# Kernel tuning notes

Hardware: AMD Instinct MI355X
Metric: run time of the kernel (lower is better)

The kernel has to match this reference:

```python
import jax, jax.numpy as jnp
import numpy as np

N = 50000
E = 600000
OB_DIM = 128
H = 128
P_OUT = 8


def _glorot(key, fan_in, fan_out):
    lim = float(np.sqrt(6.0 / (fan_in + fan_out)))
    return jax.random.uniform(key, (fan_in, fan_out), jnp.float32, -lim, lim)


def setup_inputs() -> dict:
    key = jax.random.key(0)
    ks = jax.random.split(key, 16)
    x = jax.random.normal(ks[0], (N, OB_DIM), jnp.float32)
    edge_index = jax.random.randint(ks[1], (2, E), 0, N, jnp.int64)
    dims = [(OB_DIM, H), (H, H), (H, P_OUT), (OB_DIM, H), (H, H), (H, 1)]
    names = ["p1", "p2", "p3", "v1", "v2", "v3"]
    inp = {"x": x, "edge_index": edge_index}
    for i, (nm, (fi, fo)) in enumerate(zip(names, dims)):
        inp["W" + nm] = _glorot(ks[2 + i], fi, fo)
        inp["b" + nm] = jnp.zeros((fo,), jnp.float32)
    return inp


def _gcn_norm(edge_index, n):
    # add self-loops, symmetric normalization deg^{-1/2} A_hat deg^{-1/2}
    loops = jnp.arange(n, dtype=edge_index.dtype)
    src = jnp.concatenate([edge_index[0], loops])
    dst = jnp.concatenate([edge_index[1], loops])
    deg = jax.ops.segment_sum(jnp.ones_like(dst, jnp.float32), dst, num_segments=n)
    dinv = jax.lax.rsqrt(jnp.maximum(deg, 1.0))
    norm = dinv[src] * dinv[dst]  # [E+N]
    return src, dst, norm


def _gcn_conv(x, W, b, src, dst, norm, n):
    h = x @ W                      # [N, out]
    msg = h[src] * norm[:, None]   # gather + scale, [E+N, out]
    out = jax.ops.segment_sum(msg, dst, num_segments=n)
    return out + b


def reference(x, edge_index, Wp1, bp1, Wp2, bp2, Wp3, bp3, Wv1, bv1, Wv2, bv2, Wv3, bv3):
    n = x.shape[0]
    src, dst, norm = _gcn_norm(edge_index, n)
    # policy branch
    a = jax.nn.relu(_gcn_conv(x, Wp1, bp1, src, dst, norm, n))
    a = jax.nn.relu(_gcn_conv(a, Wp2, bp2, src, dst, norm, n))
    action_logits = _gcn_conv(a, Wp3, bp3, src, dst, norm, n)  # Categorical logits
    # value branch
    v = jax.nn.relu(_gcn_conv(x, Wv1, bv1, src, dst, norm, n))
    v = jax.nn.relu(_gcn_conv(v, Wv2, bv2, src, dst, norm, n))
    v = _gcn_conv(v, Wv3, bv3, src, dst, norm, n)
    return action_logits, v
```

## Files before the change

### kernel.cpp

```cpp
#include <hip/hip_runtime.h>

#define NN 50000
#define NE 600000

typedef unsigned short ushort_t;
typedef ushort_t ushortx8 __attribute__((ext_vector_type(8)));
typedef ushort_t ushortx4 __attribute__((ext_vector_type(4)));
typedef short bf16x8 __attribute__((ext_vector_type(8)));
typedef float f32x4 __attribute__((ext_vector_type(4)));
typedef int intx2 __attribute__((ext_vector_type(2)));
typedef float fltx4 __attribute__((ext_vector_type(4)));

__device__ __forceinline__ float bf2f(ushort_t u) {
    union { unsigned int i; float f; } c;
    c.i = ((unsigned int)u) << 16;
    return c.f;
}
__device__ __forceinline__ ushort_t f2bf(float f) {
    union { float f; unsigned int i; } c;
    c.f = f;
    unsigned int u = c.i;
    unsigned int r = u + 0x7FFFu + ((u >> 16) & 1u);
    return (ushort_t)(r >> 16);
}
__device__ __forceinline__ unsigned cvtpk(float lo, float hi) {
    unsigned r;
    asm("v_cvt_pk_bf16_f32 %0, %1, %2" : "=v"(r) : "v"(lo), "v"(hi));
    return r;
}

__global__ void k_xbf(const float* __restrict__ X, ushort_t* __restrict__ XB) {
    size_t i = (size_t)blockIdx.x * 256 + threadIdx.x;
    const float4* X4 = (const float4*)X;
    float4 a = X4[i * 2], b = X4[i * 2 + 1];
    union { unsigned u[4]; ushortx8 v; } cv;
    cv.u[0] = cvtpk(a.x, a.y);
    cv.u[1] = cvtpk(a.z, a.w);
    cv.u[2] = cvtpk(b.x, b.y);
    cv.u[3] = cvtpk(b.z, b.w);
    __builtin_nontemporal_store(cv.v, (ushortx8*)XB + i);
}


__global__ void k_count(const int* __restrict__ ei, int* __restrict__ cnt) {
    int e = blockIdx.x * 256 + threadIdx.x;
    if (e < NE) {
        int d = __builtin_nontemporal_load(ei + NE + e);
        atomicAdd(&cnt[d], 1);
    }
}

__global__ void k_scan1(const int* __restrict__ cnt, int* __restrict__ rowptr,
                        int* __restrict__ bsum, float* __restrict__ dinv) {
    __shared__ int s[256];
    int t = threadIdx.x;
    int i = blockIdx.x * 256 + t;
    int v = (i < NN) ? cnt[i] : 0;
    if (i < NN) dinv[i] = rsqrtf(1.0f + (float)v);
    s[t] = v;
    __syncthreads();
    for (int d = 1; d < 256; d <<= 1) {
        int tmp = (t >= d) ? s[t - d] : 0;
        __syncthreads();
        s[t] += tmp;
        __syncthreads();
    }
    if (i < NN) rowptr[i] = s[t] - v;
    if (t == 255) bsum[blockIdx.x] = s[255];
}

__global__ void k_scan2_prep(int* __restrict__ bsum, int* __restrict__ boff, int nb,
                             const float* __restrict__ Wp1, const float* __restrict__ Wv1,
                             const float* __restrict__ Wp2, const float* __restrict__ Wv2,
                             ushort_t* __restrict__ Wt1, ushort_t* __restrict__ Wt2p,
                             ushort_t* __restrict__ Wt2v) {
    int b = blockIdx.x, t = threadIdx.x;
    if (b < 128) {
        int idx = b * 256 + t;
        int n = idx >> 7, k = idx & 127;
        float v = (n < 128) ? Wp1[k * 128 + n] : Wv1[k * 128 + (n - 128)];
        Wt1[n * 128 + k] = f2bf(v);
    } else if (b < 192) {
        int idx = (b - 128) * 256 + t;
        int n = idx >> 7, k = idx & 127;
        Wt2p[n * 128 + k] = f2bf(Wp2[k * 128 + n]);
    } else if (b < 256) {
        int idx = (b - 192) * 256 + t;
        int n = idx >> 7, k = idx & 127;
        Wt2v[n * 128 + k] = f2bf(Wv2[k * 128 + n]);
    } else {
        __shared__ int s[256];
        int v = (t < nb) ? bsum[t] : 0;
        s[t] = v;
        __syncthreads();
        for (int d = 1; d < 256; d <<= 1) {
            int tmp = (t >= d) ? s[t - d] : 0;
            __syncthreads();
            s[t] += tmp;
            __syncthreads();
        }
        boff[t] = s[t] - v;
    }
}

__global__ void k_scan3rc(const int* __restrict__ rowptr, const int* __restrict__ cnt,
                          const int* __restrict__ boff, int2* __restrict__ rc) {
    int i = blockIdx.x * 256 + threadIdx.x;
    if (i < NN) {
        int2 v;
        v.x = rowptr[i] + boff[blockIdx.x];
        v.y = cnt[i];
        rc[i] = v;
    }
}

__global__ void k_fill(const int* __restrict__ ei, const int2* __restrict__ rc,
                       int* __restrict__ fill, const float* __restrict__ dinv,
                       int2* __restrict__ edges) {
    int e = blockIdx.x * 256 + threadIdx.x;
    if (e < NE) {
        int s = __builtin_nontemporal_load(ei + e);
        int d = __builtin_nontemporal_load(ei + NE + e);
        int pos = rc[d].x + atomicAdd(&fill[d], 1);
        int2 pr;
        pr.x = s;
        pr.y = __float_as_int(dinv[s] * dinv[d]);
        edges[pos] = pr;
    }
}

__global__ __launch_bounds__(256) void k_agg128(const ushort_t* __restrict__ H,
                                                ushort_t* __restrict__ OUT,
                                                const float* __restrict__ dinv,
                                                const int2* __restrict__ rc,
                                                const int2* __restrict__ edges) {
    int wv = threadIdx.x >> 6;
    int l = threadIdx.x & 63;
    int i = blockIdx.x * 4 + wv;
    if (i >= NN) return;
    int t2 = l >> 4, q = l & 15;
    const ushortx8* H8 = (const ushortx8*)H;

    float a0[8] = {}, a1[8] = {};
    float di = dinv[i];
    float ws = (t2 == 0) ? di * di : 0.f;
    ushortx8 hv = H8[(size_t)i * 16 + q];
#pragma unroll
    for (int k = 0; k < 8; ++k) a0[k] = ws * bf2f(hv[k]);

    int2 rcv = rc[i];
    int st = rcv.x, n = rcv.y;

    for (int j = t2; j < n; j += 16) {
        int idx[4];
        float w[4];
#pragma unroll
        for (int s = 0; s < 4; ++s) {
            int jj = j + 4 * s;
            bool valid = jj < n;
            intx2 em = __builtin_nontemporal_load(
                (const intx2*)edges + (valid ? st + jj : st));
            idx[s] = valid ? em.x : i;
            w[s] = valid ? __int_as_float(em.y) : 0.f;
        }
        ushortx8 hh[4];
#pragma unroll
        for (int s = 0; s < 4; ++s) hh[s] = H8[(size_t)idx[s] * 16 + q];
#pragma unroll
        for (int k = 0; k < 8; ++k) a0[k] += w[0] * bf2f(hh[0][k]);
#pragma unroll
        for (int k = 0; k < 8; ++k) a1[k] += w[1] * bf2f(hh[1][k]);
#pragma unroll
        for (int k = 0; k < 8; ++k) a0[k] += w[2] * bf2f(hh[2][k]);
#pragma unroll
        for (int k = 0; k < 8; ++k) a1[k] += w[3] * bf2f(hh[3][k]);
    }
#pragma unroll
    for (int k = 0; k < 8; ++k) a0[k] += a1[k];
#pragma unroll
    for (int k = 0; k < 8; ++k) {
        a0[k] += __shfl_xor(a0[k], 16, 64);
        a0[k] += __shfl_xor(a0[k], 32, 64);
    }
    if (l < 16) {
        ushortx8 o = {f2bf(a0[0]), f2bf(a0[1]), f2bf(a0[2]), f2bf(a0[3]),
                      f2bf(a0[4]), f2bf(a0[5]), f2bf(a0[6]), f2bf(a0[7])};
        __builtin_nontemporal_store(o, (ushortx8*)OUT + (size_t)i * 16 + q);
    }
}

__global__ __launch_bounds__(256) void k_agg256(const ushort_t* __restrict__ H,
                                                ushort_t* __restrict__ OUT,
                                                const float* __restrict__ dinv,
                                                const int2* __restrict__ rc,
                                                const int2* __restrict__ edges) {
    int wv = threadIdx.x >> 6;
    int l = threadIdx.x & 63;
    int i = blockIdx.x * 4 + wv;
    if (i >= NN) return;
    int h = l >> 5, q = l & 31;
    const ushortx8* H8 = (const ushortx8*)H;

    float a0[8] = {}, a1[8] = {};
    float di = dinv[i];
    float ws = (h == 0) ? di * di : 0.f;
    ushortx8 hv = H8[(size_t)i * 32 + q];
#pragma unroll
    for (int k = 0; k < 8; ++k) a0[k] = ws * bf2f(hv[k]);

    int2 rcv = rc[i];
    int st = rcv.x, n = rcv.y;

    for (int j = h; j < n; j += 8) {
        int idx[4];
        float w[4];
#pragma unroll
        for (int s = 0; s < 4; ++s) {
            int jj = j + 2 * s;
            bool valid = jj < n;
            intx2 em = __builtin_nontemporal_load(
                (const intx2*)edges + (valid ? st + jj : st));
            idx[s] = valid ? em.x : i;
            w[s] = valid ? __int_as_float(em.y) : 0.f;
        }
        ushortx8 hh[4];
#pragma unroll
        for (int s = 0; s < 4; ++s) hh[s] = H8[(size_t)idx[s] * 32 + q];
#pragma unroll
        for (int k = 0; k < 8; ++k) a0[k] += w[0] * bf2f(hh[0][k]);
#pragma unroll
        for (int k = 0; k < 8; ++k) a1[k] += w[1] * bf2f(hh[1][k]);
#pragma unroll
        for (int k = 0; k < 8; ++k) a0[k] += w[2] * bf2f(hh[2][k]);
#pragma unroll
        for (int k = 0; k < 8; ++k) a1[k] += w[3] * bf2f(hh[3][k]);
    }
#pragma unroll
    for (int k = 0; k < 8; ++k) a0[k] += a1[k];
#pragma unroll
    for (int k = 0; k < 8; ++k) a0[k] += __shfl_xor(a0[k], 32, 64);

    if (h == 0) {
        ushortx8 o = {f2bf(a0[0]), f2bf(a0[1]), f2bf(a0[2]), f2bf(a0[3]),
                      f2bf(a0[4]), f2bf(a0[5]), f2bf(a0[6]), f2bf(a0[7])};
        __builtin_nontemporal_store(o, (ushortx8*)OUT + (size_t)i * 32 + q);
    }
}

__global__ __launch_bounds__(256) void k_gemm1(const ushort_t* __restrict__ A,
                                               const ushort_t* __restrict__ Wt1,
                                               const float* __restrict__ bL,
                                               const float* __restrict__ bH,
                                               ushort_t* __restrict__ C, int nrows) {
    __shared__ ushort_t Wl[256 * 128];
    int t = threadIdx.x;
    const ushortx8* Wg = (const ushortx8*)Wt1;
#pragma unroll
    for (int i = 0; i < 16; ++i) {
        int c = i * 256 + t;
        int row = c >> 4, slot = c & 15;
        int db = row * 256 + ((slot * 16) ^ ((row & 7) << 4));
        *(ushortx8*)((char*)Wl + db) = Wg[c];
    }
    __syncthreads();

    int w = t >> 6, l = t & 63, m = l & 15, g = l >> 4;
    int r0 = blockIdx.x * 64 + w * 16;
    if (r0 >= nrows) return;

    const ushort_t* Arow = A + (size_t)(r0 + m) * 128;
    bf16x8 af[4];
#pragma unroll
    for (int kk = 0; kk < 4; ++kk) af[kk] = *(const bf16x8*)(Arow + kk * 32 + g * 8);

    f32x4 acc[16];
#pragma unroll
    for (int nt = 0; nt < 16; ++nt) acc[nt] = (f32x4){0.f, 0.f, 0.f, 0.f};
    int sw = (m & 7) << 4;
#pragma unroll
    for (int nt = 0; nt < 16; ++nt) {
        const char* Wb = (const char*)Wl + (nt * 16 + m) * 256;
#pragma unroll
        for (int kk = 0; kk < 4; ++kk) {
            bf16x8 wf = *(const bf16x8*)(Wb + ((kk * 64 + g * 16) ^ sw));
            acc[nt] = __builtin_amdgcn_mfma_f32_16x16x32_bf16(wf, af[kk], acc[nt], 0, 0, 0);
        }
    }
#pragma unroll
    for (int nt = 0; nt < 16; ++nt) {
        const float* bb = (nt < 8) ? (bL + nt * 16 + g * 4) : (bH + (nt - 8) * 16 + g * 4);
        float4 bv = *(const float4*)bb;
        ushortx4 o = {f2bf(fmaxf(acc[nt][0] + bv.x, 0.f)),
                      f2bf(fmaxf(acc[nt][1] + bv.y, 0.f)),
                      f2bf(fmaxf(acc[nt][2] + bv.z, 0.f)),
                      f2bf(fmaxf(acc[nt][3] + bv.w, 0.f))};
        *(ushortx4*)(C + (size_t)(r0 + m) * 256 + nt * 16 + g * 4) = o;
    }
}

__global__ __launch_bounds__(256) void k_gemm2(const ushort_t* __restrict__ A,
                                               const ushort_t* __restrict__ Wp,
                                               const ushort_t* __restrict__ Wv,
                                               const float* __restrict__ bL,
                                               const float* __restrict__ bH,
                                               ushort_t* __restrict__ C, int nrows) {
    __shared__ ushort_t Wl[2 * 128 * 128];
    int t = threadIdx.x;
    const ushortx8* Wgp = (const ushortx8*)Wp;
    const ushortx8* Wgv = (const ushortx8*)Wv;
#pragma unroll
    for (int i = 0; i < 8; ++i) {
        int c = i * 256 + t;
        int row = c >> 4, slot = c & 15;
        int db = row * 256 + ((slot * 16) ^ ((row & 7) << 4));
        *(ushortx8*)((char*)Wl + db) = Wgp[c];
        *(ushortx8*)((char*)Wl + 32768 + db) = Wgv[c];
    }
    __syncthreads();

    int w = t >> 6, l = t & 63, m = l & 15, g = l >> 4;
    int r0 = blockIdx.x * 64 + w * 16;
    if (r0 >= nrows) return;

    const ushort_t* Arow = A + (size_t)(r0 + m) * 256;
    bf16x8 alo[4], ahi[4];
#pragma unroll
    for (int kk = 0; kk < 4; ++kk) {
        alo[kk] = *(const bf16x8*)(Arow + kk * 32 + g * 8);
        ahi[kk] = *(const bf16x8*)(Arow + 128 + kk * 32 + g * 8);
    }

    f32x4 accp[8], accv[8];
#pragma unroll
    for (int nt = 0; nt < 8; ++nt) {
        accp[nt] = (f32x4){0.f, 0.f, 0.f, 0.f};
        accv[nt] = (f32x4){0.f, 0.f, 0.f, 0.f};
    }
    int sw = (m & 7) << 4;
#pragma unroll
    for (int nt = 0; nt < 8; ++nt) {
        const char* Wbp = (const char*)Wl + (nt * 16 + m) * 256;
        const char* Wbv = Wbp + 32768;
#pragma unroll
        for (int kk = 0; kk < 4; ++kk) {
            int off = (kk * 64 + g * 16) ^ sw;
            bf16x8 wfp = *(const bf16x8*)(Wbp + off);
            accp[nt] = __builtin_amdgcn_mfma_f32_16x16x32_bf16(wfp, alo[kk], accp[nt], 0, 0, 0);
            bf16x8 wfv = *(const bf16x8*)(Wbv + off);
            accv[nt] = __builtin_amdgcn_mfma_f32_16x16x32_bf16(wfv, ahi[kk], accv[nt], 0, 0, 0);
        }
    }
#pragma unroll
    for (int nt = 0; nt < 8; ++nt) {
        float4 bp = *(const float4*)(bL + nt * 16 + g * 4);
        float4 bv = *(const float4*)(bH + nt * 16 + g * 4);
        ushortx4 op = {f2bf(fmaxf(accp[nt][0] + bp.x, 0.f)),
                       f2bf(fmaxf(accp[nt][1] + bp.y, 0.f)),
                       f2bf(fmaxf(accp[nt][2] + bp.z, 0.f)),
                       f2bf(fmaxf(accp[nt][3] + bp.w, 0.f))};
        ushortx4 ov = {f2bf(fmaxf(accv[nt][0] + bv.x, 0.f)),
                       f2bf(fmaxf(accv[nt][1] + bv.y, 0.f)),
                       f2bf(fmaxf(accv[nt][2] + bv.z, 0.f)),
                       f2bf(fmaxf(accv[nt][3] + bv.w, 0.f))};
        *(ushortx4*)(C + (size_t)(r0 + m) * 256 + nt * 16 + g * 4) = op;
        *(ushortx4*)(C + (size_t)(r0 + m) * 256 + 128 + nt * 16 + g * 4) = ov;
    }
}

__global__ __launch_bounds__(256) void k_small(const ushort_t* __restrict__ F2,
                                               const float* __restrict__ Wp3,
                                               const float* __restrict__ Wv3,
                                               float* __restrict__ FS) {
    __shared__ float Wp[8 * 128];
    __shared__ float Wv[128];
    int t = threadIdx.x;
    for (int j = t; j < 1024; j += 256) {
        int k = j >> 3, c = j & 7;
        Wp[c * 128 + k] = Wp3[j];
    }
    if (t < 128) Wv[t] = Wv3[t];
    __syncthreads();
    int row = blockIdx.x * 256 + t;
    if (row >= NN) return;
    const ushortx8* F8 = (const ushortx8*)F2;
    size_t base = (size_t)row * 32;
    float acc[9] = {};
#pragma unroll 2
    for (int kc = 0; kc < 16; ++kc) {
        ushortx8 p = F8[base + kc];
        ushortx8 v = F8[base + 16 + kc];
#pragma unroll
        for (int jj = 0; jj < 8; ++jj) {
            float pv = bf2f(p[jj]);
            int k = kc * 8 + jj;
#pragma unroll
            for (int c = 0; c < 8; ++c) acc[c] += pv * Wp[c * 128 + k];
            acc[8] += bf2f(v[jj]) * Wv[k];
        }
    }
    float4* FSo = (float4*)(FS + (size_t)row * 12);
    float4 o0 = {acc[0], acc[1], acc[2], acc[3]};
    float4 o1 = {acc[4], acc[5], acc[6], acc[7]};
    float4 o2 = {acc[8], 0.f, 0.f, 0.f};
    FSo[0] = o0; FSo[1] = o1; FSo[2] = o2;
}

__global__ void k_agg9(const float* __restrict__ FS, float* __restrict__ out_logits,
                       float* __restrict__ out_v, const float* __restrict__ bp3,
                       const float* __restrict__ bv3, const float* __restrict__ dinv,
                       const int2* __restrict__ rc, const int2* __restrict__ edges) {
    int i = blockIdx.x * 256 + threadIdx.x;
    if (i >= NN) return;
    float di = dinv[i];
    float w0 = di * di;
    const float4* F = (const float4*)FS;
    size_t b0 = (size_t)i * 3;
    float4 x0 = F[b0], x1 = F[b0 + 1], x2 = F[b0 + 2];
    float a[9];
    a[0] = w0 * x0.x; a[1] = w0 * x0.y; a[2] = w0 * x0.z; a[3] = w0 * x0.w;
    a[4] = w0 * x1.x; a[5] = w0 * x1.y; a[6] = w0 * x1.z; a[7] = w0 * x1.w;
    a[8] = w0 * x2.x;
    int2 rcv = rc[i];
    int st = rcv.x, n = rcv.y;
    for (int j = 0; j < n; ++j) {
        int2 e = edges[st + j];
        float w = __int_as_float(e.y);
        size_t sb = (size_t)e.x * 3;
        float4 y0 = F[sb], y1 = F[sb + 1], y2 = F[sb + 2];
        a[0] += w * y0.x; a[1] += w * y0.y; a[2] += w * y0.z; a[3] += w * y0.w;
        a[4] += w * y1.x; a[5] += w * y1.y; a[6] += w * y1.z; a[7] += w * y1.w;
        a[8] += w * y2.x;
    }
    float4 bpa = *(const float4*)bp3;
    float4 bpb = *(const float4*)(bp3 + 4);
    fltx4 o0 = {a[0] + bpa.x, a[1] + bpa.y, a[2] + bpa.z, a[3] + bpa.w};
    fltx4 o1 = {a[4] + bpb.x, a[5] + bpb.y, a[6] + bpb.z, a[7] + bpb.w};
    __builtin_nontemporal_store(o0, (fltx4*)out_logits + (size_t)i * 2);
    __builtin_nontemporal_store(o1, (fltx4*)out_logits + (size_t)i * 2 + 1);
    __builtin_nontemporal_store(a[8] + bv3[0], out_v + i);
}

extern "C" void kernel_launch(void* const* d_in, const int* in_sizes, int n_in,
                              void* d_out, int out_size, void* d_ws, size_t ws_size,
                              hipStream_t stream) {
    const float* x   = (const float*)d_in[0];
    const int*   ei  = (const int*)d_in[1];
    const float* Wp1 = (const float*)d_in[2],  *bp1 = (const float*)d_in[3];
    const float* Wp2 = (const float*)d_in[4],  *bp2 = (const float*)d_in[5];
    const float* Wp3 = (const float*)d_in[6],  *bp3 = (const float*)d_in[7];
    const float* Wv1 = (const float*)d_in[8],  *bv1 = (const float*)d_in[9];
    const float* Wv2 = (const float*)d_in[10], *bv2 = (const float*)d_in[11];
    const float* Wv3 = (const float*)d_in[12], *bv3 = (const float*)d_in[13];
    float* out_logits = (float*)d_out;
    float* out_v = (float*)d_out + (size_t)NN * 8;

    char* w = (char*)d_ws;
    auto alloc = [&](size_t bytes) {
        char* p = w;
        w += (bytes + 255) & ~(size_t)255;
        return p;
    };
    int*      cntfill = (int*)alloc((size_t)2 * NN * 4);
    int*      cnt    = cntfill;
    int*      fill   = cntfill + NN;
    int*      rowptr = (int*)alloc(NN * 4);
    int*      bsum   = (int*)alloc(256 * 4);
    int*      boff   = (int*)alloc(256 * 4);
    float*    dinv   = (float*)alloc(NN * 4);
    int2*     rc     = (int2*)alloc((size_t)NN * 8);
    int2*     edges  = (int2*)alloc((size_t)NE * 8);
    ushort_t* Wt1    = (ushort_t*)alloc(256 * 128 * 2);
    ushort_t* Wt2p   = (ushort_t*)alloc(128 * 128 * 2);
    ushort_t* Wt2v   = (ushort_t*)alloc(128 * 128 * 2);
    ushort_t* xb     = (ushort_t*)alloc((size_t)NN * 128 * 2);
    ushort_t* ag0    = (ushort_t*)alloc((size_t)NN * 128 * 2);
    ushort_t* f1b    = (ushort_t*)alloc((size_t)NN * 256 * 2);
    ushort_t* ag1    = (ushort_t*)alloc((size_t)NN * 256 * 2);
    ushort_t* f2b    = (ushort_t*)alloc((size_t)NN * 256 * 2);
    float*    fs     = (float*)alloc((size_t)NN * 12 * 4);

    const int NB = (NN + 255) / 256;
    const int EB = (NE + 255) / 256;
    const int GB = (NN + 63) / 64;
    const int AB = NN / 4;

    k_xbf<<<3125, 256, 0, stream>>>(x, xb);
    (void)hipMemsetAsync(cntfill, 0, (size_t)2 * NN * 4, stream);
    k_count<<<EB, 256, 0, stream>>>(ei, cnt);
    k_scan1<<<NB, 256, 0, stream>>>(cnt, rowptr, bsum, dinv);
    k_scan2_prep<<<257, 256, 0, stream>>>(bsum, boff, NB, Wp1, Wv1, Wp2, Wv2,
                                          Wt1, Wt2p, Wt2v);
    k_scan3rc<<<NB, 256, 0, stream>>>(rowptr, cnt, boff, rc);
    k_fill<<<EB, 256, 0, stream>>>(ei, rc, fill, dinv, edges);

    k_agg128<<<AB, 256, 0, stream>>>(xb, ag0, dinv, rc, edges);
    k_gemm1<<<GB, 256, 0, stream>>>(ag0, Wt1, bp1, bv1, f1b, NN);
    k_agg256<<<AB, 256, 0, stream>>>(f1b, ag1, dinv, rc, edges);
    k_gemm2<<<GB, 256, 0, stream>>>(ag1, Wt2p, Wt2v, bp2, bv2, f2b, NN);
    k_small<<<NB, 256, 0, stream>>>(f2b, Wp3, Wv3, fs);
    k_agg9<<<NB, 256, 0, stream>>>(fs, out_logits, out_v, bp3, bv3, dinv, rc, edges);
}
```

Measured before the change: 219.3 us.

## Fuse final small GEMM into gemm2, merge preprocessing kernels, compact edge list

```diff
diff --git a/kernel.cpp b/kernel.cpp
--- a/kernel.cpp
+++ b/kernel.cpp
@@ -8,7 +8,6 @@
 typedef ushort_t ushortx4 __attribute__((ext_vector_type(4)));
 typedef short bf16x8 __attribute__((ext_vector_type(8)));
 typedef float f32x4 __attribute__((ext_vector_type(4)));
-typedef int intx2 __attribute__((ext_vector_type(2)));
 typedef float fltx4 __attribute__((ext_vector_type(4)));
 
 __device__ __forceinline__ float bf2f(ushort_t u) {
@@ -29,24 +28,25 @@
     return r;
 }
 
-__global__ void k_xbf(const float* __restrict__ X, ushort_t* __restrict__ XB) {
-    size_t i = (size_t)blockIdx.x * 256 + threadIdx.x;
-    const float4* X4 = (const float4*)X;
-    float4 a = X4[i * 2], b = X4[i * 2 + 1];
-    union { unsigned u[4]; ushortx8 v; } cv;
-    cv.u[0] = cvtpk(a.x, a.y);
-    cv.u[1] = cvtpk(a.z, a.w);
-    cv.u[2] = cvtpk(b.x, b.y);
-    cv.u[3] = cvtpk(b.z, b.w);
-    __builtin_nontemporal_store(cv.v, (ushortx8*)XB + i);
-}
-
-
-__global__ void k_count(const int* __restrict__ ei, int* __restrict__ cnt) {
-    int e = blockIdx.x * 256 + threadIdx.x;
-    if (e < NE) {
-        int d = __builtin_nontemporal_load(ei + NE + e);
-        atomicAdd(&cnt[d], 1);
+__global__ void k_pre(const float* __restrict__ X, ushort_t* __restrict__ XB,
+                      const int* __restrict__ ei, int* __restrict__ cnt) {
+    int b = blockIdx.x;
+    if (b < 3125) {
+        size_t i = (size_t)b * 256 + threadIdx.x;
+        const float4* X4 = (const float4*)X;
+        float4 a = X4[i * 2], c4 = X4[i * 2 + 1];
+        union { unsigned u[4]; ushortx8 v; } cv;
+        cv.u[0] = cvtpk(a.x, a.y);
+        cv.u[1] = cvtpk(a.z, a.w);
+        cv.u[2] = cvtpk(c4.x, c4.y);
+        cv.u[3] = cvtpk(c4.z, c4.w);
+        __builtin_nontemporal_store(cv.v, (ushortx8*)XB + i);
+    } else {
+        int e = (b - 3125) * 256 + threadIdx.x;
+        if (e < NE) {
+            int d = __builtin_nontemporal_load(ei + NE + e);
+            atomicAdd(&cnt[d], 1);
+        }
     }
 }
 
@@ -115,17 +115,13 @@
 }
 
 __global__ void k_fill(const int* __restrict__ ei, const int2* __restrict__ rc,
-                       int* __restrict__ fill, const float* __restrict__ dinv,
-                       int2* __restrict__ edges) {
+                       int* __restrict__ fill, int* __restrict__ edges) {
     int e = blockIdx.x * 256 + threadIdx.x;
     if (e < NE) {
         int s = __builtin_nontemporal_load(ei + e);
         int d = __builtin_nontemporal_load(ei + NE + e);
         int pos = rc[d].x + atomicAdd(&fill[d], 1);
-        int2 pr;
-        pr.x = s;
-        pr.y = __float_as_int(dinv[s] * dinv[d]);
-        edges[pos] = pr;
+        edges[pos] = s;
     }
 }
 
@@ -133,7 +129,7 @@
                                                 ushort_t* __restrict__ OUT,
                                                 const float* __restrict__ dinv,
                                                 const int2* __restrict__ rc,
-                                                const int2* __restrict__ edges) {
+                                                const int* __restrict__ edges) {
     int wv = threadIdx.x >> 6;
     int l = threadIdx.x & 63;
     int i = blockIdx.x * 4 + wv;
@@ -158,10 +154,9 @@
         for (int s = 0; s < 4; ++s) {
             int jj = j + 4 * s;
             bool valid = jj < n;
-            intx2 em = __builtin_nontemporal_load(
-                (const intx2*)edges + (valid ? st + jj : st));
-            idx[s] = valid ? em.x : i;
-            w[s] = valid ? __int_as_float(em.y) : 0.f;
+            int em = __builtin_nontemporal_load(edges + (valid ? st + jj : st));
+            idx[s] = valid ? em : i;
+            w[s] = valid ? dinv[em] * di : 0.f;
         }
         ushortx8 hh[4];
 #pragma unroll
@@ -193,7 +188,7 @@
                                                 ushort_t* __restrict__ OUT,
                                                 const float* __restrict__ dinv,
                                                 const int2* __restrict__ rc,
-                                                const int2* __restrict__ edges) {
+                                                const int* __restrict__ edges) {
     int wv = threadIdx.x >> 6;
     int l = threadIdx.x & 63;
     int i = blockIdx.x * 4 + wv;
@@ -218,10 +213,9 @@
         for (int s = 0; s < 4; ++s) {
             int jj = j + 2 * s;
             bool valid = jj < n;
-            intx2 em = __builtin_nontemporal_load(
-                (const intx2*)edges + (valid ? st + jj : st));
-            idx[s] = valid ? em.x : i;
-            w[s] = valid ? __int_as_float(em.y) : 0.f;
+            int em = __builtin_nontemporal_load(edges + (valid ? st + jj : st));
+            idx[s] = valid ? em : i;
+            w[s] = valid ? dinv[em] * di : 0.f;
         }
         ushortx8 hh[4];
 #pragma unroll
@@ -298,13 +292,16 @@
     }
 }
 
-__global__ __launch_bounds__(256) void k_gemm2(const ushort_t* __restrict__ A,
-                                               const ushort_t* __restrict__ Wp,
-                                               const ushort_t* __restrict__ Wv,
-                                               const float* __restrict__ bL,
-                                               const float* __restrict__ bH,
-                                               ushort_t* __restrict__ C, int nrows) {
+__global__ __launch_bounds__(256) void k_gemm2s(const ushort_t* __restrict__ A,
+                                                const ushort_t* __restrict__ Wp,
+                                                const ushort_t* __restrict__ Wv,
+                                                const float* __restrict__ bL,
+                                                const float* __restrict__ bH,
+                                                const float* __restrict__ Wp3,
+                                                const float* __restrict__ Wv3,
+                                                float* __restrict__ FS, int nrows) {
     __shared__ ushort_t Wl[2 * 128 * 128];
+    __shared__ float W3c[9][128];
     int t = threadIdx.x;
     const ushortx8* Wgp = (const ushortx8*)Wp;
     const ushortx8* Wgv = (const ushortx8*)Wv;
@@ -316,6 +313,10 @@
         *(ushortx8*)((char*)Wl + db) = Wgp[c];
         *(ushortx8*)((char*)Wl + 32768 + db) = Wgv[c];
     }
+    for (int jj = t; jj < 1152; jj += 256) {
+        int c = jj >> 7, k = jj & 127;
+        W3c[c][k] = (c < 8) ? Wp3[k * 8 + c] : Wv3[k];
+    }
     __syncthreads();
 
     int w = t >> 6, l = t & 63, m = l & 15, g = l >> 4;
@@ -350,65 +351,55 @@
             accv[nt] = __builtin_amdgcn_mfma_f32_16x16x32_bf16(wfv, ahi[kk], accv[nt], 0, 0, 0);
         }
     }
+
+    float rp[8][4], rv[8][4];
 #pragma unroll
     for (int nt = 0; nt < 8; ++nt) {
         float4 bp = *(const float4*)(bL + nt * 16 + g * 4);
         float4 bv = *(const float4*)(bH + nt * 16 + g * 4);
-        ushortx4 op = {f2bf(fmaxf(accp[nt][0] + bp.x, 0.f)),
-                       f2bf(fmaxf(accp[nt][1] + bp.y, 0.f)),
-                       f2bf(fmaxf(accp[nt][2] + bp.z, 0.f)),
-                       f2bf(fmaxf(accp[nt][3] + bp.w, 0.f))};
-        ushortx4 ov = {f2bf(fmaxf(accv[nt][0] + bv.x, 0.f)),
-                       f2bf(fmaxf(accv[nt][1] + bv.y, 0.f)),
-                       f2bf(fmaxf(accv[nt][2] + bv.z, 0.f)),
-                       f2bf(fmaxf(accv[nt][3] + bv.w, 0.f))};
-        *(ushortx4*)(C + (size_t)(r0 + m) * 256 + nt * 16 + g * 4) = op;
-        *(ushortx4*)(C + (size_t)(r0 + m) * 256 + 128 + nt * 16 + g * 4) = ov;
-    }
-}
-
-__global__ __launch_bounds__(256) void k_small(const ushort_t* __restrict__ F2,
-                                               const float* __restrict__ Wp3,
-                                               const float* __restrict__ Wv3,
-                                               float* __restrict__ FS) {
-    __shared__ float Wp[8 * 128];
-    __shared__ float Wv[128];
-    int t = threadIdx.x;
-    for (int j = t; j < 1024; j += 256) {
-        int k = j >> 3, c = j & 7;
-        Wp[c * 128 + k] = Wp3[j];
-    }
-    if (t < 128) Wv[t] = Wv3[t];
-    __syncthreads();
-    int row = blockIdx.x * 256 + t;
-    if (row >= NN) return;
-    const ushortx8* F8 = (const ushortx8*)F2;
-    size_t base = (size_t)row * 32;
-    float acc[9] = {};
-#pragma unroll 2
-    for (int kc = 0; kc < 16; ++kc) {
-        ushortx8 p = F8[base + kc];
-        ushortx8 v = F8[base + 16 + kc];
-#pragma unroll
-        for (int jj = 0; jj < 8; ++jj) {
-            float pv = bf2f(p[jj]);
-            int k = kc * 8 + jj;
-#pragma unroll
-            for (int c = 0; c < 8; ++c) acc[c] += pv * Wp[c * 128 + k];
-            acc[8] += bf2f(v[jj]) * Wv[k];
-        }
-    }
-    float4* FSo = (float4*)(FS + (size_t)row * 12);
-    float4 o0 = {acc[0], acc[1], acc[2], acc[3]};
-    float4 o1 = {acc[4], acc[5], acc[6], acc[7]};
-    float4 o2 = {acc[8], 0.f, 0.f, 0.f};
-    FSo[0] = o0; FSo[1] = o1; FSo[2] = o2;
+        rp[nt][0] = fmaxf(accp[nt][0] + bp.x, 0.f);
+        rp[nt][1] = fmaxf(accp[nt][1] + bp.y, 0.f);
+        rp[nt][2] = fmaxf(accp[nt][2] + bp.z, 0.f);
+        rp[nt][3] = fmaxf(accp[nt][3] + bp.w, 0.f);
+        rv[nt][0] = fmaxf(accv[nt][0] + bv.x, 0.f);
+        rv[nt][1] = fmaxf(accv[nt][1] + bv.y, 0.f);
+        rv[nt][2] = fmaxf(accv[nt][2] + bv.z, 0.f);
+        rv[nt][3] = fmaxf(accv[nt][3] + bv.w, 0.f);
+    }
+
+    float ps[9] = {};
+#pragma unroll
+    for (int c = 0; c < 8; ++c) {
+#pragma unroll
+        for (int nt = 0; nt < 8; ++nt) {
+            float4 w4 = *(const float4*)&W3c[c][nt * 16 + g * 4];
+            ps[c] += rp[nt][0] * w4.x + rp[nt][1] * w4.y + rp[nt][2] * w4.z + rp[nt][3] * w4.w;
+        }
+    }
+#pragma unroll
+    for (int nt = 0; nt < 8; ++nt) {
+        float4 w4 = *(const float4*)&W3c[8][nt * 16 + g * 4];
+        ps[8] += rv[nt][0] * w4.x + rv[nt][1] * w4.y + rv[nt][2] * w4.z + rv[nt][3] * w4.w;
+    }
+#pragma unroll
+    for (int c = 0; c < 9; ++c) {
+        ps[c] += __shfl_xor(ps[c], 16, 64);
+        ps[c] += __shfl_xor(ps[c], 32, 64);
+    }
+    if (g == 0) {
+        float* o = FS + (size_t)(r0 + m) * 12;
+        fltx4 o0 = {ps[0], ps[1], ps[2], ps[3]};
+        fltx4 o1 = {ps[4], ps[5], ps[6], ps[7]};
+        __builtin_nontemporal_store(o0, (fltx4*)o);
+        __builtin_nontemporal_store(o1, (fltx4*)o + 1);
+        __builtin_nontemporal_store(ps[8], o + 8);
+    }
 }
 
 __global__ void k_agg9(const float* __restrict__ FS, float* __restrict__ out_logits,
                        float* __restrict__ out_v, const float* __restrict__ bp3,
                        const float* __restrict__ bv3, const float* __restrict__ dinv,
-                       const int2* __restrict__ rc, const int2* __restrict__ edges) {
+                       const int2* __restrict__ rc, const int* __restrict__ edges) {
     int i = blockIdx.x * 256 + threadIdx.x;
     if (i >= NN) return;
     float di = dinv[i];
@@ -423,9 +414,9 @@
     int2 rcv = rc[i];
     int st = rcv.x, n = rcv.y;
     for (int j = 0; j < n; ++j) {
-        int2 e = edges[st + j];
-        float w = __int_as_float(e.y);
-        size_t sb = (size_t)e.x * 3;
+        int e = edges[st + j];
+        float w = dinv[e] * di;
+        size_t sb = (size_t)e * 3;
         float4 y0 = F[sb], y1 = F[sb + 1], y2 = F[sb + 2];
         a[0] += w * y0.x; a[1] += w * y0.y; a[2] += w * y0.z; a[3] += w * y0.w;
         a[4] += w * y1.x; a[5] += w * y1.y; a[6] += w * y1.z; a[7] += w * y1.w;
@@ -468,7 +459,7 @@
     int*      boff   = (int*)alloc(256 * 4);
     float*    dinv   = (float*)alloc(NN * 4);
     int2*     rc     = (int2*)alloc((size_t)NN * 8);
-    int2*     edges  = (int2*)alloc((size_t)NE * 8);
+    int*      edges  = (int*)alloc((size_t)NE * 4);
     ushort_t* Wt1    = (ushort_t*)alloc(256 * 128 * 2);
     ushort_t* Wt2p   = (ushort_t*)alloc(128 * 128 * 2);
     ushort_t* Wt2v   = (ushort_t*)alloc(128 * 128 * 2);
@@ -476,7 +467,6 @@
     ushort_t* ag0    = (ushort_t*)alloc((size_t)NN * 128 * 2);
     ushort_t* f1b    = (ushort_t*)alloc((size_t)NN * 256 * 2);
     ushort_t* ag1    = (ushort_t*)alloc((size_t)NN * 256 * 2);
-    ushort_t* f2b    = (ushort_t*)alloc((size_t)NN * 256 * 2);
     float*    fs     = (float*)alloc((size_t)NN * 12 * 4);
 
     const int NB = (NN + 255) / 256;
@@ -484,19 +474,17 @@
     const int GB = (NN + 63) / 64;
     const int AB = NN / 4;
 
-    k_xbf<<<3125, 256, 0, stream>>>(x, xb);
     (void)hipMemsetAsync(cntfill, 0, (size_t)2 * NN * 4, stream);
-    k_count<<<EB, 256, 0, stream>>>(ei, cnt);
+    k_pre<<<3125 + EB, 256, 0, stream>>>(x, xb, ei, cnt);
     k_scan1<<<NB, 256, 0, stream>>>(cnt, rowptr, bsum, dinv);
     k_scan2_prep<<<257, 256, 0, stream>>>(bsum, boff, NB, Wp1, Wv1, Wp2, Wv2,
                                           Wt1, Wt2p, Wt2v);
     k_scan3rc<<<NB, 256, 0, stream>>>(rowptr, cnt, boff, rc);
-    k_fill<<<EB, 256, 0, stream>>>(ei, rc, fill, dinv, edges);
+    k_fill<<<EB, 256, 0, stream>>>(ei, rc, fill, edges);
 
     k_agg128<<<AB, 256, 0, stream>>>(xb, ag0, dinv, rc, edges);
     k_gemm1<<<GB, 256, 0, stream>>>(ag0, Wt1, bp1, bv1, f1b, NN);
     k_agg256<<<AB, 256, 0, stream>>>(f1b, ag1, dinv, rc, edges);
-    k_gemm2<<<GB, 256, 0, stream>>>(ag1, Wt2p, Wt2v, bp2, bv2, f2b, NN);
-    k_small<<<NB, 256, 0, stream>>>(f2b, Wp3, Wv3, fs);
+    k_gemm2s<<<GB, 256, 0, stream>>>(ag1, Wt2p, Wt2v, bp2, bv2, Wp3, Wv3, fs, NN);
     k_agg9<<<NB, 256, 0, stream>>>(fs, out_logits, out_v, bp3, bv3, dinv, rc, edges);
 }
```

After: 229.5 us. +4.6%, slower.
